# Optimization experiments

Hardware: AMD Instinct MI355X
Metric: run time of the kernel (lower is better)

Reference implementation:

```python
import jax, jax.numpy as jnp
import numpy as np

N = 10000
E = 320000
H = 4
D = 64
C = 16
IN = 256


def setup_inputs() -> dict:
    key = jax.random.key(0)
    ks = jax.random.split(key, 10)
    h = jax.random.normal(ks[0], (N, IN), dtype=jnp.float32)
    logits = jax.random.normal(ks[1], (N, C), dtype=jnp.float32)
    old_z = jax.random.uniform(ks[2], (N, H), dtype=jnp.float32)
    attn_l = jax.random.normal(ks[3], (1, H, D), dtype=jnp.float32) * 0.1
    attn_r = jax.random.normal(ks[4], (1, H, D), dtype=jnp.float32) * 0.1
    Wfc = jax.random.normal(ks[5], (IN, H * D), dtype=jnp.float32) * (1.0 / np.sqrt(IN))
    tau1 = jnp.full((1,), 0.5, dtype=jnp.float32)
    tau2 = jnp.full((1,), 0.5, dtype=jnp.float32)
    src = jax.random.randint(ks[6], (E,), 0, N, dtype=jnp.int32)
    dst = jax.random.randint(ks[7], (E,), 0, N, dtype=jnp.int32)
    return {"h": h, "logits": logits, "old_z": old_z, "attn_l": attn_l,
            "attn_r": attn_r, "Wfc": Wfc, "tau1": tau1, "tau2": tau2,
            "src": src, "dst": dst}


def _layernorm_all(x, eps=1e-5):
    # LayerNorm((num_nodes, num_heads), elementwise_affine=False):
    # normalizes over the entire [N, H] tensor jointly.
    mu = jnp.mean(x)
    var = jnp.mean((x - mu) ** 2)
    return (x - mu) * jax.lax.rsqrt(var + eps)


def reference(h, logits, old_z, attn_l, attn_r, Wfc, tau1, tau2, src, dst):
    n = h.shape[0]
    # fc projection -> [N, H, D] (dropout=0.0 -> identity)
    feat = (h @ Wfc).reshape(n, H, D)

    # in-degrees, clamped to >= 1; symmetric-norm factor
    ones_e = jnp.ones((src.shape[0],), dtype=feat.dtype)
    degs = jnp.clip(jax.ops.segment_sum(ones_e, dst, num_segments=n), 1.0)  # [N]
    norm = degs ** -0.5  # [N]

    # GAT attention logits
    el = jnp.sum(feat * attn_l, axis=-1)  # [N, H]
    er = jnp.sum(feat * attn_r, axis=-1)  # [N, H]
    e = el[src] + er[dst]                 # [E, H]
    e = jnp.where(e > 0, e, 0.2 * e)      # leaky_relu(0.2)

    # edge softmax over incoming edges of each dst node
    emax = jax.ops.segment_max(e, dst, num_segments=n)      # [N, H]
    eexp = jnp.exp(e - emax[dst])                           # [E, H]
    denom = jax.ops.segment_sum(eexp, dst, num_segments=n)  # [N, H]
    a = eexp / denom[dst]                                   # [E, H]

    # mailbox consistency (f1) and entropy (f2) features (detached)
    pred = jnp.argmax(logits, axis=-1)          # [N]
    edge_pred = pred[src]                       # [E]
    match = (edge_pred == pred[dst]).astype(a.dtype)  # [E]
    f1 = jax.ops.segment_sum(a * match[:, None], dst, num_segments=n) / degs[:, None]  # [N, H]

    onehot = jax.nn.one_hot(edge_pred, C, dtype=a.dtype)  # [E, C]
    cnts = jax.ops.segment_sum(a[:, :, None] * onehot[:, None, :], dst, num_segments=n)
    cnts = jnp.clip(cnts / degs[:, None, None], 1e-5)     # [N, H, C]
    # original loops over unique(pred): only classes present among edge preds
    present = (jnp.sum(onehot, axis=0) > 0).astype(a.dtype)  # [C]
    f2 = -jnp.sum(present * cnts * jnp.log(cnts), axis=-1)   # [N, H]

    f1 = jax.lax.stop_gradient(f1)
    f2 = jax.lax.stop_gradient(f2)

    norm_f1 = _layernorm_all(f1)
    norm_f2 = _layernorm_all(f2)
    # shared_tau=True path: uses tau1/tau2 passed to forward
    z = jax.nn.sigmoid(tau1 - norm_f1) * jax.nn.sigmoid(tau2 - norm_f2)  # [N, H]
    gate = jnp.minimum(old_z, z)

    # attention-weighted neighbor aggregation
    agg = jax.ops.segment_sum(feat[src] * a[:, :, None], dst, num_segments=n)  # [N, H, D]
    normagg = agg * norm[:, None, None]
    new_h = feat + gate[:, :, None] * normagg
    return new_h, z
```

## Files before the change

### kernel.cpp

```cpp
#include <hip/hip_runtime.h>
#include <math.h>

constexpr int NN = 10000;
constexpr int EE = 320000;
constexpr int H  = 4;
constexpr int D  = 64;
constexpr int C  = 16;
constexpr int IN = 256;
constexpr int HD = H * D;
constexpr int STRIDE = 128;
constexpr int NBKT = 64;

typedef __attribute__((ext_vector_type(8))) short bf16x8;
typedef __attribute__((ext_vector_type(4))) float f32x4;

__device__ __forceinline__ unsigned short f2b(float x) {
    unsigned int b = __float_as_uint(x);
    return (unsigned short)((b + 0x7FFFu + ((b >> 16) & 1u)) >> 16);
}
__device__ __forceinline__ float b2f(unsigned short u) {
    return __uint_as_float((unsigned int)u << 16);
}

constexpr long OFF_FB   = 0;
constexpr long OFF_EL   = OFF_FB   + (long)NN * HD / 2;
constexpr long OFF_ER   = OFF_EL   + (long)NN * H;
constexpr long OFF_F1   = OFF_ER   + (long)NN * H;
constexpr long OFF_F2   = OFF_F1   + (long)NN * H;
constexpr long OFF_AGGB = OFF_F2   + (long)NN * H;
constexpr long OFF_PRED = OFF_AGGB + (long)NN * HD / 2;
constexpr long OFF_SSRC = OFF_PRED + (long)NN;
constexpr long OFF_DEGI = OFF_SSRC + (long)NN * STRIDE;
constexpr long OFF_BKT  = OFF_DEGI + (long)NN;
constexpr long OFF_WP   = (OFF_BKT + NBKT * 4 + 3) & ~3L;
constexpr long WS_END   = OFF_WP + 32768;

constexpr int GEMB = NN / 16;
constexpr int PB   = (NN + 255) / 256;
constexpr int CB   = (EE + 255) / 256;
constexpr int ZB   = (NN + 255) / 256;

__global__ __launch_bounds__(256) void k_pack(const float* __restrict__ W,
                                              const float* __restrict__ logits,
                                              unsigned short* __restrict__ wp,
                                              int* __restrict__ pred,
                                              int* __restrict__ deg_i,
                                              float* __restrict__ bkt) {
    int bid = blockIdx.x;
    int t = threadIdx.x;
    if (bid < 32) {
        int tg = bid * 256 + t;
        int l  = tg & 63;
        int ct = (tg >> 6) & 3;
        int ks = (tg >> 8) & 7;
        int w  = tg >> 11;
        int col = w * 64 + ct * 16 + (l & 15);
        int kb  = ks * 32 + (l >> 4) * 8;
        unsigned short v[8];
#pragma unroll
        for (int i = 0; i < 8; ++i) v[i] = f2b(W[(long)(kb + i) * HD + col]);
        ushort4* p = (ushort4*)(wp + (long)tg * 8);
        p[0] = make_ushort4(v[0], v[1], v[2], v[3]);
        p[1] = make_ushort4(v[4], v[5], v[6], v[7]);
    } else if (bid < 32 + ZB) {
        int n = (bid - 32) * 256 + t;
        if (n < NN) deg_i[n] = 0;
        if (bid == 32) bkt[t] = 0.f;
    } else {
        int n = (bid - 32 - ZB) * 256 + t;
        if (n < NN) {
            const float* row = logits + (long)n * C;
            float best = row[0]; int bi = 0;
#pragma unroll
            for (int c = 1; c < C; ++c) { float v = row[c]; if (v > best) { best = v; bi = c; } }
            pred[n] = bi;
        }
    }
}

__global__ __launch_bounds__(256) void k_main(const float* __restrict__ hin,
                                              const unsigned short* __restrict__ wp,
                                              const float* __restrict__ al,
                                              const float* __restrict__ ar,
                                              const int*   __restrict__ src,
                                              const int*   __restrict__ dst,
                                              const int*   __restrict__ pred,
                                              unsigned short* __restrict__ featb,
                                              float* __restrict__ el,
                                              float* __restrict__ er,
                                              int*   __restrict__ deg_i,
                                              int*   __restrict__ ssrc) {
    int bid = blockIdx.x;
    int t = threadIdx.x;
    if (bid < GEMB) {
        int tile = bid;
        int w = t >> 6, l = t & 63;
        int g = l >> 4, fr = l & 15;

        f32x4 acc[4];
#pragma unroll
        for (int ct = 0; ct < 4; ++ct) acc[ct] = (f32x4){0.f, 0.f, 0.f, 0.f};

        const unsigned short* wpw = wp + (long)w * 8 * 4 * 64 * 8;
        const float* hrow = hin + (long)(tile * 16 + fr) * IN + g * 8;

        for (int ks = 0; ks < 8; ++ks) {
            float4 a0 = *(const float4*)(hrow + ks * 32);
            float4 a1 = *(const float4*)(hrow + ks * 32 + 4);
            bf16x8 af;
            af[0] = (short)f2b(a0.x); af[1] = (short)f2b(a0.y);
            af[2] = (short)f2b(a0.z); af[3] = (short)f2b(a0.w);
            af[4] = (short)f2b(a1.x); af[5] = (short)f2b(a1.y);
            af[6] = (short)f2b(a1.z); af[7] = (short)f2b(a1.w);
#pragma unroll
            for (int ct = 0; ct < 4; ++ct) {
                bf16x8 bfr = *(const bf16x8*)(wpw + (((long)ks * 4 + ct) * 64 + l) * 8);
                acc[ct] = __builtin_amdgcn_mfma_f32_16x16x32_bf16(af, bfr, acc[ct], 0, 0, 0);
            }
        }

        float aLr[4], aRr[4];
#pragma unroll
        for (int ct = 0; ct < 4; ++ct) {
            aLr[ct] = al[w * 64 + ct * 16 + fr];
            aRr[ct] = ar[w * 64 + ct * 16 + fr];
        }
#pragma unroll
        for (int j = 0; j < 4; ++j) {
            int row = tile * 16 + g * 4 + j;
            float vl = 0.f, vr = 0.f;
#pragma unroll
            for (int ct = 0; ct < 4; ++ct) {
                float v = acc[ct][j];
                featb[(long)row * HD + w * 64 + ct * 16 + fr] = f2b(v);
                vl = fmaf(v, aLr[ct], vl);
                vr = fmaf(v, aRr[ct], vr);
            }
            vl += __shfl_xor(vl, 1); vl += __shfl_xor(vl, 2);
            vl += __shfl_xor(vl, 4); vl += __shfl_xor(vl, 8);
            vr += __shfl_xor(vr, 1); vr += __shfl_xor(vr, 2);
            vr += __shfl_xor(vr, 4); vr += __shfl_xor(vr, 8);
            if (fr == 0) {
                el[(long)row * H + w] = vl;
                er[(long)row * H + w] = vr;
            }
        }
    } else {
        int e = (bid - GEMB) * 256 + t;
        if (e < EE) {
            int s = src[e];
            int d = dst[e];
            int r = atomicAdd(&deg_i[d], 1);
            ssrc[(long)d * STRIDE + r] = s | (pred[s] << 16);
        }
    }
}

#define EDGE(st, kk) { \
    int spk = __builtin_amdgcn_readlane(spreg[st], (kk)); \
    int s_  = spk & 0xFFFF; \
    int ps_ = spk >> 16; \
    float wa = __shfl(wreg[st], (hidx << 4) | (kk)); \
    const ushort4 f = *(const ushort4*)(featb + (long)s_ * HD + (lane << 2)); \
    acc.x = fmaf(wa, b2f(f.x), acc.x); \
    acc.y = fmaf(wa, b2f(f.y), acc.y); \
    acc.z = fmaf(wa, b2f(f.z), acc.z); \
    acc.w = fmaf(wa, b2f(f.w), acc.w); \
    f1a += (ps_ == pd)   ? wa : 0.f; \
    ca  += (ps_ == cidx) ? wa : 0.f; \
}

__global__ __launch_bounds__(256) void k_agg(const int* __restrict__ deg_i,
                                             const int* __restrict__ ssrc,
                                             const float* __restrict__ el,
                                             const float* __restrict__ er,
                                             const unsigned short* __restrict__ featb,
                                             const int* __restrict__ pred,
                                             unsigned short* __restrict__ aggb,
                                             float* __restrict__ f1,
                                             float* __restrict__ f2,
                                             float* __restrict__ bkt) {
    __shared__ float red[4][4];
    int lane = threadIdx.x & 63;
    int wv = threadIdx.x >> 6;
    int n = blockIdx.x * 4 + wv;
    int deg = deg_i[n];
    long beg = (long)n * STRIDE;
    int hidx = lane >> 4, cidx = lane & 15;
    float Rh = er[(long)n * H + hidx];
    int pd = pred[n];
    int nst = (deg + 15) >> 4;

    float wreg[8]; int spreg[8];
    float dsum = 0.f;
#pragma unroll
    for (int st = 0; st < 8; ++st) {
        wreg[st] = 0.f; spreg[st] = 0;
        int idx = st * 16 + cidx;
        if (st < nst && idx < deg) {
            int sp = ssrc[beg + idx];
            int s = sp & 0xFFFF;
            float x = el[(long)s * H + hidx] + Rh;
            x = x > 0.f ? x : 0.2f * x;
            wreg[st] = __expf(x);
            spreg[st] = sp;
        }
        dsum += wreg[st];
    }

    float4 acc = {0.f, 0.f, 0.f, 0.f};
    float f1a = 0.f, ca = 0.f;
#pragma unroll
    for (int st = 0; st < 8; ++st) {
        if (st >= nst) break;
#pragma unroll
        for (int k = 0; k < 16; ++k) EDGE(st, k)
    }

    for (int off = 1; off < 16; off <<= 1) dsum += __shfl_xor(dsum, off);
    float invh = dsum > 0.f ? 1.f / dsum : 0.f;
    float invdeg = 1.0f / (float)(deg > 0 ? deg : 1);

    ushort4 ob = make_ushort4(f2b(acc.x * invh), f2b(acc.y * invh),
                              f2b(acc.z * invh), f2b(acc.w * invh));
    *(ushort4*)(aggb + (long)n * HD + (lane << 2)) = ob;

    float f1v = f1a * invh * invdeg;
    float v = fmaxf(ca * invh * invdeg, 1e-5f);
    float term = -v * logf(v);
    for (int off = 1; off < 16; off <<= 1) term += __shfl_xor(term, off);
    if (cidx == 0) {
        f1[(long)n * H + hidx] = f1v;
        f2[(long)n * H + hidx] = term;
    }

    float c1 = (cidx == 0) ? f1v : 0.f;
    float c2 = (cidx == 0) ? term : 0.f;
    float q1 = c1 * f1v, q2 = c2 * term;
    for (int off = 1; off < 64; off <<= 1) {
        c1 += __shfl_xor(c1, off);
        q1 += __shfl_xor(q1, off);
        c2 += __shfl_xor(c2, off);
        q2 += __shfl_xor(q2, off);
    }
    if (lane == 0) { red[wv][0] = c1; red[wv][1] = q1; red[wv][2] = c2; red[wv][3] = q2; }
    __syncthreads();
    if (threadIdx.x < 4) {
        float a = red[0][threadIdx.x] + red[1][threadIdx.x]
                + red[2][threadIdx.x] + red[3][threadIdx.x];
        atomicAdd(&bkt[(blockIdx.x & (NBKT - 1)) * 4 + threadIdx.x], a);
    }
}

__global__ __launch_bounds__(256) void k_out(const unsigned short* __restrict__ featb,
                                             const unsigned short* __restrict__ aggb,
                                             const float* __restrict__ f1,
                                             const float* __restrict__ f2,
                                             const float* __restrict__ bkt,
                                             const float* __restrict__ old_z,
                                             const float* __restrict__ tau1,
                                             const float* __restrict__ tau2,
                                             const int* __restrict__ deg_i,
                                             float* __restrict__ out,
                                             float* __restrict__ zout) {
    __shared__ float sred[4];
    int lane = threadIdx.x & 63;
    int wv = threadIdx.x >> 6;
    float pv = bkt[lane * 4 + wv];
    for (int off = 1; off < 64; off <<= 1) pv += __shfl_xor(pv, off);
    if (lane == 0) sred[wv] = pv;
    __syncthreads();

    long i4 = ((long)blockIdx.x * 256 + threadIdx.x) * 4;
    if (i4 >= (long)NN * HD) return;
    int n = (int)(i4 >> 8);
    int h = (int)((i4 >> 6) & 3);
    int t = n * H + h;
    constexpr float invNH = 1.0f / (NN * H);
    float mu1 = sred[0] * invNH, mu2 = sred[2] * invNH;
    float v1 = fmaxf(sred[1] * invNH - mu1 * mu1, 0.f);
    float v2 = fmaxf(sred[3] * invNH - mu2 * mu2, 0.f);
    float r1 = rsqrtf(v1 + 1e-5f), r2 = rsqrtf(v2 + 1e-5f);
    float nf1 = (f1[t] - mu1) * r1;
    float nf2 = (f2[t] - mu2) * r2;
    float z = (1.f / (1.f + expf(nf1 - tau1[0]))) * (1.f / (1.f + expf(nf2 - tau2[0])));
    float gate = fminf(old_z[t], z);
    if ((i4 & 63) == 0) zout[t] = z;
    int deg = deg_i[n];
    float g = gate * rsqrtf((float)(deg > 0 ? deg : 1));
    const ushort4 fb = *(const ushort4*)(featb + i4);
    const ushort4 ag = *(const ushort4*)(aggb + i4);
    float4 o;
    o.x = fmaf(g, b2f(ag.x), b2f(fb.x));
    o.y = fmaf(g, b2f(ag.y), b2f(fb.y));
    o.z = fmaf(g, b2f(ag.z), b2f(fb.z));
    o.w = fmaf(g, b2f(ag.w), b2f(fb.w));
    *(float4*)(out + i4) = o;
}

extern "C" void kernel_launch(void* const* d_in, const int* in_sizes, int n_in,
                              void* d_out, int out_size, void* d_ws, size_t ws_size,
                              hipStream_t stream) {
    const float* hin    = (const float*)d_in[0];
    const float* logits = (const float*)d_in[1];
    const float* old_z  = (const float*)d_in[2];
    const float* attn_l = (const float*)d_in[3];
    const float* attn_r = (const float*)d_in[4];
    const float* Wfc    = (const float*)d_in[5];
    const float* tau1   = (const float*)d_in[6];
    const float* tau2   = (const float*)d_in[7];
    const int*   src    = (const int*)d_in[8];
    const int*   dst    = (const int*)d_in[9];
    float* out = (float*)d_out;
    float* ws  = (float*)d_ws;

    unsigned short* featb = (unsigned short*)(ws + OFF_FB);
    unsigned short* aggb  = (unsigned short*)(ws + OFF_AGGB);
    unsigned short* wp    = (unsigned short*)(ws + OFF_WP);
    int* pred   = (int*)(ws + OFF_PRED);
    int* ssrc   = (int*)(ws + OFF_SSRC);
    int* deg_i  = (int*)(ws + OFF_DEGI);
    float* bkt  = ws + OFF_BKT;

    k_pack <<<32 + ZB + PB, 256, 0, stream>>>(Wfc, logits, wp, pred, deg_i, bkt);
    k_main <<<GEMB + CB, 256, 0, stream>>>(hin, wp, attn_l, attn_r,
                                           src, dst, pred, featb,
                                           ws + OFF_EL, ws + OFF_ER,
                                           deg_i, ssrc);
    k_agg  <<<NN / 4, 256, 0, stream>>>(deg_i, ssrc, ws + OFF_EL, ws + OFF_ER,
                                        featb, pred, aggb,
                                        ws + OFF_F1, ws + OFF_F2, bkt);
    k_out  <<<(NN * HD / 4 + 255) / 256, 256, 0, stream>>>(featb, aggb,
                                                           ws + OFF_F1, ws + OFF_F2, bkt,
                                                           old_z, tau1, tau2, deg_i,
                                                           out, out + (long)NN * HD);
}
```

Measured before the change: 66.66 us.

## Gather two edges per wave with 16-byte loads and LDS class histogram

The aggregation loop now has each half-wave handle a different edge, with each lane loading 8 bf16 features (16 bytes) instead of 4. The two halves are combined at the end with a cross-half shuffle. This halves the number of serialized gather iterations per node. The f1 and class-count accumulations move out of the inner loop into the weight-computation phase, using an LDS histogram built with shared atomics. The risks are LDS atomic contention and the use of chist without an explicit barrier between zeroing and use, which relies on wave-local ordering.

```diff
diff --git a/kernel.cpp b/kernel.cpp
--- a/kernel.cpp
+++ b/kernel.cpp
@@ -13,6 +13,7 @@
 
 typedef __attribute__((ext_vector_type(8))) short bf16x8;
 typedef __attribute__((ext_vector_type(4))) float f32x4;
+typedef __attribute__((ext_vector_type(8))) unsigned short u16x8;
 
 __device__ __forceinline__ unsigned short f2b(float x) {
     unsigned int b = __float_as_uint(x);
@@ -156,18 +157,21 @@
     }
 }
 
-#define EDGE(st, kk) { \
-    int spk = __builtin_amdgcn_readlane(spreg[st], (kk)); \
-    int s_  = spk & 0xFFFF; \
-    int ps_ = spk >> 16; \
-    float wa = __shfl(wreg[st], (hidx << 4) | (kk)); \
-    const ushort4 f = *(const ushort4*)(featb + (long)s_ * HD + (lane << 2)); \
-    acc.x = fmaf(wa, b2f(f.x), acc.x); \
-    acc.y = fmaf(wa, b2f(f.y), acc.y); \
-    acc.z = fmaf(wa, b2f(f.z), acc.z); \
-    acc.w = fmaf(wa, b2f(f.w), acc.w); \
-    f1a += (ps_ == pd)   ? wa : 0.f; \
-    ca  += (ps_ == cidx) ? wa : 0.f; \
+#define EDGE2(st, kk) { \
+    int sp0 = __builtin_amdgcn_readlane(spreg[st], (kk)); \
+    int sp1 = __builtin_amdgcn_readlane(spreg[st], (kk) + 1); \
+    int sph = half ? sp1 : sp0; \
+    int s_  = sph & 0xFFFF; \
+    float wa = __shfl(wreg[st], (chead << 4) | ((kk) + half)); \
+    const u16x8 f = *(const u16x8*)(featb + (long)s_ * HD + jj * 8); \
+    acc[0] = fmaf(wa, b2f(f[0]), acc[0]); \
+    acc[1] = fmaf(wa, b2f(f[1]), acc[1]); \
+    acc[2] = fmaf(wa, b2f(f[2]), acc[2]); \
+    acc[3] = fmaf(wa, b2f(f[3]), acc[3]); \
+    acc[4] = fmaf(wa, b2f(f[4]), acc[4]); \
+    acc[5] = fmaf(wa, b2f(f[5]), acc[5]); \
+    acc[6] = fmaf(wa, b2f(f[6]), acc[6]); \
+    acc[7] = fmaf(wa, b2f(f[7]), acc[7]); \
 }
 
 __global__ __launch_bounds__(256) void k_agg(const int* __restrict__ deg_i,
@@ -181,18 +185,23 @@
                                              float* __restrict__ f2,
                                              float* __restrict__ bkt) {
     __shared__ float red[4][4];
+    __shared__ float chist[4][64];
     int lane = threadIdx.x & 63;
     int wv = threadIdx.x >> 6;
     int n = blockIdx.x * 4 + wv;
     int deg = deg_i[n];
     long beg = (long)n * STRIDE;
     int hidx = lane >> 4, cidx = lane & 15;
+    int half = lane >> 5, jj = lane & 31;
+    int chead = jj >> 3;
     float Rh = er[(long)n * H + hidx];
     int pd = pred[n];
     int nst = (deg + 15) >> 4;
 
+    chist[wv][lane] = 0.f;
+
     float wreg[8]; int spreg[8];
-    float dsum = 0.f;
+    float dsum = 0.f, f1a = 0.f;
 #pragma unroll
     for (int st = 0; st < 8; ++st) {
         wreg[st] = 0.f; spreg[st] = 0;
@@ -200,32 +209,47 @@
         if (st < nst && idx < deg) {
             int sp = ssrc[beg + idx];
             int s = sp & 0xFFFF;
+            int ps = sp >> 16;
             float x = el[(long)s * H + hidx] + Rh;
             x = x > 0.f ? x : 0.2f * x;
-            wreg[st] = __expf(x);
-            spreg[st] = sp;
+            float w = __expf(x);
+            wreg[st] = w;
+            spreg[st] = (hidx == 0) ? sp : 0;
+            f1a += (ps == pd) ? w : 0.f;
+            atomicAdd(&chist[wv][(hidx << 4) | ps], w);
         }
         dsum += wreg[st];
     }
 
-    float4 acc = {0.f, 0.f, 0.f, 0.f};
-    float f1a = 0.f, ca = 0.f;
+    float acc[8];
+#pragma unroll
+    for (int i = 0; i < 8; ++i) acc[i] = 0.f;
 #pragma unroll
     for (int st = 0; st < 8; ++st) {
         if (st >= nst) break;
 #pragma unroll
-        for (int k = 0; k < 16; ++k) EDGE(st, k)
-    }
-
-    for (int off = 1; off < 16; off <<= 1) dsum += __shfl_xor(dsum, off);
+        for (int k = 0; k < 16; k += 2) EDGE2(st, k)
+    }
+#pragma unroll
+    for (int i = 0; i < 8; ++i) acc[i] += __shfl_xor(acc[i], 32);
+
+    for (int off = 1; off < 16; off <<= 1) {
+        dsum += __shfl_xor(dsum, off);
+        f1a  += __shfl_xor(f1a, off);
+    }
     float invh = dsum > 0.f ? 1.f / dsum : 0.f;
     float invdeg = 1.0f / (float)(deg > 0 ? deg : 1);
 
-    ushort4 ob = make_ushort4(f2b(acc.x * invh), f2b(acc.y * invh),
-                              f2b(acc.z * invh), f2b(acc.w * invh));
-    *(ushort4*)(aggb + (long)n * HD + (lane << 2)) = ob;
+    float invw = __shfl(invh, chead << 4);
+    if (half == 0) {
+        u16x8 ob;
+#pragma unroll
+        for (int i = 0; i < 8; ++i) ob[i] = f2b(acc[i] * invw);
+        *(u16x8*)(aggb + (long)n * HD + jj * 8) = ob;
+    }
 
     float f1v = f1a * invh * invdeg;
+    float ca = chist[wv][lane];
     float v = fmaxf(ca * invh * invdeg, 1e-5f);
     float term = -v * logf(v);
     for (int off = 1; off < 16; off <<= 1) term += __shfl_xor(term, off);
```

Result: faster. 63.55 us (-4.7%).
